# Kernel tuning notes

Hardware: AMD Instinct MI355X
Metric: run time of the kernel (lower is better)

Reference implementation:

```python
import jax, jax.numpy as jnp
import numpy as np

B = 8192          # batch_size = len(embedds)
D = 512           # ll_p['num_channels'][-1]
C = 100           # n_classes
N_LAB = 4096      # int(B * plb), plb = 0.5
MAX_ITER = 30     # gtg_i
TOL = 1e-3        # gtg_t
ENT_EPS = 1e-20


def _mlp(x, W1, b1, W2, b2, W3, b3, Wc, bc):
    h = jax.nn.relu(x @ W1 + b1)
    h = jax.nn.relu(h @ W2 + b2)
    h = jax.nn.relu(h @ W3 + b3)
    return (h @ Wc + bc)[:, 0]  # squeeze -> [B]


def _entropy(X):
    # per-row Shannon entropy (bits), as in ALGTG utils
    return -jnp.sum(X * jnp.log2(X + ENT_EPS), axis=1)


def _gtg_entropy_hist(embedds, labels):
    # get_A: cos_sim -> zero diagonal -> clamp [0,1] -> 'mean' threshold -> 'diversity' (1-A)
    n = jnp.maximum(jnp.linalg.norm(embedds, axis=-1, keepdims=True), 1e-12)
    E = embedds / n
    A = E @ E.T                                   # [B,B]
    A = A * (1.0 - jnp.eye(B, dtype=A.dtype))     # fill_diagonal_(0)
    A = jnp.clip(A, 0.0, 1.0)
    A = jnp.where(A < jnp.mean(A), 0.0, A)        # AM_threshold_strategy == 'mean'
    A = 1.0 - A                                   # AM_strategy == 'diversity'

    # get_X: labeled rows one-hot, unlabeled rows uniform 1/C
    lab = jnp.arange(B) < N_LAB
    X0 = jnp.where(lab[:, None],
                   jax.nn.one_hot(labels, C, dtype=jnp.float32),
                   jnp.full((B, C), 1.0 / C, jnp.float32))
    hist0 = jnp.zeros((B, MAX_ITER), jnp.float32)
    unlab = ~lab

    def cond(s):
        _X, _h, i, err = s
        return (err > TOL) & (i < MAX_ITER)

    def body(s):
        X, hist, i, _err = s
        Xn = X * (A @ X)                          # replicator dynamics step
        Xn = Xn / jnp.sum(Xn, axis=1, keepdims=True)
        ent = _entropy(Xn)
        hist = hist.at[:, i].set(jnp.where(unlab, ent, 0.0))
        return (Xn, hist, i + 1, jnp.linalg.norm(Xn - X))

    init = (X0, hist0, jnp.array(0, jnp.int32), jnp.array(jnp.inf, jnp.float32))
    _, hist, _, _ = jax.lax.while_loop(cond, body, init)
    return hist


def setup_inputs() -> dict:
    key = jax.random.key(0)
    ks = jax.random.split(key, 11)
    d2, d4, d8 = D // 2, D // 4, D // 8

    def lin(k, fi, fo):
        return jax.random.normal(k, (fi, fo), jnp.float32) / np.float32(np.sqrt(fi))

    return {
        'features': jax.random.normal(ks[0], (B, 64), jnp.float32),
        'embedds': jax.random.normal(ks[1], (B, D), jnp.float32),
        'labels': jax.random.randint(ks[2], (B,), 0, C),
        'W1': lin(ks[3], D, d2), 'b1': jnp.zeros((d2,), jnp.float32),
        'W2': lin(ks[4], d2, d4), 'b2': jnp.zeros((d4,), jnp.float32),
        'W3': lin(ks[5], d4, d8), 'b3': jnp.zeros((d8,), jnp.float32),
        'Wc': lin(ks[6], d8, 1), 'bc': jnp.zeros((1,), jnp.float32),
    }


def reference(features, embedds, labels, W1, b1, W2, b2, W3, b3, Wc, bc):
    y_pred = _mlp(embedds, W1, b1, W2, b2, W3, b3, Wc, bc)        # [B]
    hist = _gtg_entropy_hist(embedds, labels)                      # [B, MAX_ITER]
    y_true = jnp.mean(hist, axis=1)                                # ent_strategy == 'mean'
    labeled_mask = jnp.arange(B) < N_LAB                           # bool [B]
    return (y_pred, y_true, labeled_mask)
```

## Files before the change

kernel.cpp:

```cpp
#include <hip/hip_runtime.h>
#include <hip/hip_bf16.h>
#include <math.h>

namespace {
constexpr int BROWS = 8192;
constexpr int NLAB  = 4096;
constexpr int NUNL  = 4096;
constexpr int CREAL = 100;
constexpr int CPAD  = 112;
constexpr int DIM   = 512;
constexpr int MAXIT = 30;

constexpr size_t MiB = 1ull << 20;
constexpr size_t OFF_S    = 0;
constexpr size_t OFF_AU   = 64 * MiB;
constexpr size_t OFF_EB   = 96 * MiB;
constexpr size_t OFF_XT0  = 96 * MiB;
constexpr size_t OFF_XT1  = 98 * MiB;
constexpr size_t OFF_XU   = 100 * MiB;
constexpr size_t OFF_PL   = 102 * MiB;
constexpr size_t OFF_HIST = 104 * MiB;
constexpr size_t OFF_ERR  = 104 * MiB + 16384;
constexpr size_t OFF_MS   = 104 * MiB + 16768;
constexpr size_t OFF_RN   = 104 * MiB + 32768;
constexpr size_t MEMSET_LEN = 20480;
}

typedef __attribute__((ext_vector_type(8))) short short8;
typedef __attribute__((ext_vector_type(4))) float floatx4;

__device__ inline ushort f2bf(float f) {
  __hip_bfloat16 h = __float2bfloat16(f);
  union { __hip_bfloat16 b; ushort u; } c; c.b = h; return c.u;
}
__device__ inline float bf2f(ushort u) {
  union { ushort u; __hip_bfloat16 b; } c; c.u = u;
  return __bfloat162float(c.b);
}

__global__ __launch_bounds__(64) void k_prep(const float* __restrict__ emb,
                                             ushort* __restrict__ Eb,
                                             float* __restrict__ rn) {
  int row = blockIdx.x, l = threadIdx.x;
  const float4* e4 = (const float4*)(emb + (size_t)row * DIM);
  float4 a = e4[2 * l], b = e4[2 * l + 1];
  float f[8] = {a.x, a.y, a.z, a.w, b.x, b.y, b.z, b.w};
  float s = 0.f;
#pragma unroll
  for (int q = 0; q < 8; q++) s += f[q] * f[q];
#pragma unroll
  for (int m = 1; m < 64; m <<= 1) s += __shfl_xor(s, m);
  if (l == 0) rn[row] = 1.0f / fmaxf(sqrtf(s), 1e-12f);
  union { short8 v; ushort u[8]; } o;
#pragma unroll
  for (int q = 0; q < 8; q++) o.u[q] = f2bf(f[q]);
  *(short8*)(Eb + (size_t)row * DIM + l * 8) = o.v;
}

__global__ __launch_bounds__(256) void k_initX(ushort* __restrict__ X0,
                                               ushort* __restrict__ X1,
                                               float* __restrict__ Xu,
                                               const int* __restrict__ labels) {
  int j = blockIdx.x * 256 + threadIdx.x;
  int c = blockIdx.y;
  float v;
  if (j < NLAB) v = (labels[j] == c) ? 1.0f : 0.0f;
  else          v = (c < CREAL) ? 0.01f : 0.0f;
  ushort b = f2bf(v);
  X0[(size_t)c * BROWS + j] = b;
  X1[(size_t)c * BROWS + j] = b;
  if (j >= NLAB) Xu[(size_t)(j - NLAB) * CPAD + c] = (c < CREAL) ? 0.01f : 0.0f;
}

__global__ __launch_bounds__(256) void k_mlp(const float* __restrict__ emb,
                                             const float* __restrict__ W1, const float* __restrict__ b1,
                                             const float* __restrict__ W2, const float* __restrict__ b2,
                                             const float* __restrict__ W3, const float* __restrict__ b3,
                                             const float* __restrict__ Wc, const float* __restrict__ bc,
                                             float* __restrict__ out) {
  __shared__ float xs[4][512];
  __shared__ float h1[4][256];
  __shared__ float h2[4][128];
  __shared__ float h3[4][64];
  int t = threadIdx.x;
  int r0 = blockIdx.x * 4;
  {
    const float4* src = (const float4*)(emb + (size_t)r0 * DIM);
    float4* dst = (float4*)&xs[0][0];
    dst[t] = src[t];
    dst[t + 256] = src[t + 256];
  }
  __syncthreads();
  {
    float a0 = 0.f, a1 = 0.f, a2 = 0.f, a3 = 0.f;
    for (int k = 0; k < 512; k++) {
      float w = W1[k * 256 + t];
      a0 = fmaf(xs[0][k], w, a0);
      a1 = fmaf(xs[1][k], w, a1);
      a2 = fmaf(xs[2][k], w, a2);
      a3 = fmaf(xs[3][k], w, a3);
    }
    float bb = b1[t];
    h1[0][t] = fmaxf(a0 + bb, 0.f);
    h1[1][t] = fmaxf(a1 + bb, 0.f);
    h1[2][t] = fmaxf(a2 + bb, 0.f);
    h1[3][t] = fmaxf(a3 + bb, 0.f);
  }
  __syncthreads();
  {
    int c = t & 127, rb = (t >> 7) * 2;
    float a0 = 0.f, a1 = 0.f;
    for (int k = 0; k < 256; k++) {
      float w = W2[k * 128 + c];
      a0 = fmaf(h1[rb][k], w, a0);
      a1 = fmaf(h1[rb + 1][k], w, a1);
    }
    float bb = b2[c];
    h2[rb][c] = fmaxf(a0 + bb, 0.f);
    h2[rb + 1][c] = fmaxf(a1 + bb, 0.f);
  }
  __syncthreads();
  {
    int c = t & 63, r = t >> 6;
    float a = 0.f;
    for (int k = 0; k < 128; k++) a = fmaf(h2[r][k], W3[k * 64 + c], a);
    h3[r][c] = fmaxf(a + b3[c], 0.f);
  }
  __syncthreads();
  {
    int r = t >> 6, l = t & 63;
    float v = h3[r][l] * Wc[l];
#pragma unroll
    for (int m = 32; m; m >>= 1) v += __shfl_down(v, m);
    if (l == 0) out[r0 + r] = v + bc[0];
  }
}

__global__ __launch_bounds__(256) void k_simM(const ushort* __restrict__ Eb,
                                              const float* __restrict__ rn,
                                              ushort* __restrict__ S,
                                              double* __restrict__ meansum) {
  int x = blockIdx.x, y = blockIdx.y;
  if (x < 32 && y > x) return;
  __shared__ float redbuf[4];

  int t = threadIdx.x;
  int w = t >> 6, lane = t & 63;
  int m = lane & 15, g = lane >> 4;
  int ib = (w >> 1) * 64, jb = (w & 1) * 64;
  int i0 = x * 128, j0 = y * 128;

  floatx4 acc[4][4];
#pragma unroll
  for (int a = 0; a < 4; a++)
#pragma unroll
    for (int b = 0; b < 4; b++) acc[a][b] = (floatx4)0.0f;

  const ushort* Ei = Eb + (size_t)(i0 + ib + m) * DIM + g * 8;
  const ushort* Ej = Eb + (size_t)(j0 + jb + m) * DIM + g * 8;

  for (int kt = 0; kt < DIM; kt += 32) {
    short8 ah[4], bh[4];
#pragma unroll
    for (int rt = 0; rt < 4; rt++) ah[rt] = *(const short8*)(Ei + (size_t)(rt * 16) * DIM + kt);
#pragma unroll
    for (int ct = 0; ct < 4; ct++) bh[ct] = *(const short8*)(Ej + (size_t)(ct * 16) * DIM + kt);
#pragma unroll
    for (int rt = 0; rt < 4; rt++)
#pragma unroll
      for (int ct = 0; ct < 4; ct++)
        acc[rt][ct] = __builtin_amdgcn_mfma_f32_16x16x32_bf16(ah[rt], bh[ct], acc[rt][ct], 0, 0, 0);
  }

  bool dostore = (x >= 32);
  bool isdiag  = (x == y);
  float weight = (x < 32) ? (isdiag ? 1.0f : 2.0f) : ((y < 32) ? 2.0f : 1.0f);
  float lsum = 0.f;
#pragma unroll
  for (int rt = 0; rt < 4; rt++) {
    int gi0 = i0 + ib + rt * 16 + g * 4;
    float4 rni = *(const float4*)(rn + gi0);
#pragma unroll
    for (int ct = 0; ct < 4; ct++) {
      int gj = j0 + jb + ct * 16 + m;
      float rnj = rn[gj];
#pragma unroll
      for (int r = 0; r < 4; r++) {
        int gi = gi0 + r;
        float rv = (r == 0) ? rni.x : (r == 1) ? rni.y : (r == 2) ? rni.z : rni.w;
        float s = acc[rt][ct][r] * rv * rnj;
        if (isdiag && gi == gj) s = 0.f;
        s = fminf(fmaxf(s, 0.f), 1.f);
        lsum += s;
        if (dostore) S[(size_t)(gi - NLAB) * BROWS + gj] = f2bf(s);
      }
    }
  }
  lsum *= weight;
#pragma unroll
  for (int d = 1; d < 64; d <<= 1) lsum += __shfl_xor(lsum, d);
  if (lane == 0) redbuf[w] = lsum;
  __syncthreads();
  if (t == 0) atomicAdd(meansum, (double)(redbuf[0] + redbuf[1] + redbuf[2] + redbuf[3]));
}

__global__ __launch_bounds__(1024, 4) void k_iter(const ushort* __restrict__ S,
                                                  ushort* __restrict__ Au,
                                                  const ushort* __restrict__ XTr,
                                                  ushort* __restrict__ XTw,
                                                  float* __restrict__ Xu,
                                                  float* __restrict__ Plab,
                                                  float* __restrict__ hist,
                                                  float* __restrict__ errsq,
                                                  const double* __restrict__ ms,
                                                  int it) {
  if (it > 0 && errsq[it - 1] <= 1e-6f) return;
  __shared__ float part[8][16 * 113];
  __shared__ float Pbuf[16 * 114];
  __shared__ float dsqbuf[16];
  int t = threadIdx.x;
  int w = t >> 6, lane = t & 63;
  int m = lane & 15, g = lane >> 4;
  int r0 = blockIdx.x * 16;

  floatx4 acc[7];
#pragma unroll
  for (int c = 0; c < 7; c++) acc[c] = (floatx4)0.0f;

  if (it == 0) {
    float mean = (float)(ms[0] * (1.0 / ((double)BROWS * (double)BROWS)));
    int kw = w * 512;
    for (int ks = 0; ks < 16; ks++) {
      int kk = kw + ks * 32;
      size_t so = (size_t)(r0 + m) * BROWS + kk + g * 8;
      short8 a = __builtin_nontemporal_load((const short8*)(S + so));
      union { short8 v; ushort u[8]; } ua; ua.v = a;
#pragma unroll
      for (int e = 0; e < 8; e++) {
        float s = bf2f(ua.u[e]);
        float av = (s < mean) ? 1.0f : 1.0f - s;
        ua.u[e] = f2bf(av);
      }
      a = ua.v;
      if (w >= 8)
        *(short8*)(Au + (size_t)(r0 + m) * NUNL + (kk - NLAB) + g * 8) = a;
#pragma unroll
      for (int ct = 0; ct < 7; ct++) {
        short8 b = *(const short8*)(XTr + (size_t)(ct * 16 + m) * BROWS + kk + g * 8);
        acc[ct] = __builtin_amdgcn_mfma_f32_16x16x32_bf16(a, b, acc[ct], 0, 0, 0);
      }
    }
  } else {
    int kw = w * 256;
    size_t abase = (size_t)(r0 + m) * NUNL + kw + g * 8;
    size_t bbase = (size_t)m * BROWS + NLAB + kw + g * 8;
    short8 aC = __builtin_nontemporal_load((const short8*)(Au + abase));
    for (int ks = 0; ks < 8; ks++) {
      short8 aN;
      if (ks < 7) aN = __builtin_nontemporal_load((const short8*)(Au + abase + (ks + 1) * 32));
#pragma unroll
      for (int ct = 0; ct < 7; ct++) {
        short8 b = *(const short8*)(XTr + bbase + (size_t)ct * 16 * BROWS + ks * 32);
        acc[ct] = __builtin_amdgcn_mfma_f32_16x16x32_bf16(aC, b, acc[ct], 0, 0, 0);
      }
      aC = aN;
    }
  }

  if (w < 8) {
#pragma unroll
    for (int ct = 0; ct < 7; ct++)
#pragma unroll
      for (int r = 0; r < 4; r++)
        part[w][(g * 4 + r) * 113 + ct * 16 + m] = acc[ct][r];
  }
  __syncthreads();
  float sA[2] = {0.f, 0.f}, sB[2] = {0.f, 0.f};
#pragma unroll
  for (int q = 0; q < 2; q++) {
    int idx = t + q * 1024;
    if (idx < 16 * CPAD) {
      int row = idx / CPAD, col = idx % CPAD;
      int o = row * 113 + col;
      sA[q] = ((part[0][o] + part[1][o]) + (part[2][o] + part[3][o]))
            + ((part[4][o] + part[5][o]) + (part[6][o] + part[7][o]));
    }
  }
  __syncthreads();
  if (w >= 8) {
#pragma unroll
    for (int ct = 0; ct < 7; ct++)
#pragma unroll
      for (int r = 0; r < 4; r++)
        part[w - 8][(g * 4 + r) * 113 + ct * 16 + m] = acc[ct][r];
  }
  __syncthreads();
#pragma unroll
  for (int q = 0; q < 2; q++) {
    int idx = t + q * 1024;
    if (idx < 16 * CPAD) {
      int row = idx / CPAD, col = idx % CPAD;
      int o = row * 113 + col;
      sB[q] = ((part[0][o] + part[1][o]) + (part[2][o] + part[3][o]))
            + ((part[4][o] + part[5][o]) + (part[6][o] + part[7][o]));
      float P;
      size_t go = (size_t)(r0 + row) * CPAD + col;
      if (it == 0) { Plab[go] = sA[q]; P = sA[q] + sB[q]; }
      else         { P = sA[q] + sB[q] + Plab[go]; }
      Pbuf[row * 114 + col] = P;
    }
  }
  __syncthreads();

  int gr = r0 + w;
  bool act = lane < 56;
  float2 p = make_float2(0.f, 0.f), xo = make_float2(0.f, 0.f);
  if (act) {
    p = *(const float2*)&Pbuf[w * 114 + lane * 2];
    xo = *(const float2*)(Xu + (size_t)gr * CPAD + lane * 2);
  }
  float2 xn;
  xn.x = xo.x * p.x;
  xn.y = xo.y * p.y;
  float s = xn.x + xn.y;
#pragma unroll
  for (int d = 1; d < 64; d <<= 1) s += __shfl_xor(s, d);
  float inv = 1.0f / s;
  float ent = 0.f, dsq = 0.f;
  if (act) {
    xn.x *= inv; xn.y *= inv;
    ent = -(xn.x * log2f(xn.x + 1e-20f) + xn.y * log2f(xn.y + 1e-20f));
    float dx = xn.x - xo.x, dy = xn.y - xo.y;
    dsq = dx * dx + dy * dy;
    *(float2*)(Xu + (size_t)gr * CPAD + lane * 2) = xn;
    int c0 = lane * 2, jg = NLAB + gr;
    XTw[(size_t)c0 * BROWS + jg]       = f2bf(xn.x);
    XTw[(size_t)(c0 + 1) * BROWS + jg] = f2bf(xn.y);
  }
#pragma unroll
  for (int d = 1; d < 64; d <<= 1) { ent += __shfl_xor(ent, d); dsq += __shfl_xor(dsq, d); }
  if (lane == 0) {
    hist[gr] += ent;
    dsqbuf[w] = dsq;
  }
  __syncthreads();
  if (t == 0) {
    float ds = 0.f;
#pragma unroll
    for (int i = 0; i < 16; i++) ds += dsqbuf[i];
    atomicAdd(&errsq[it], ds);
  }
}

__global__ __launch_bounds__(256) void k_final(const float* __restrict__ hist,
                                               float* __restrict__ out) {
  int i = blockIdx.x * 256 + threadIdx.x;
  float yt = (i < NLAB) ? 0.0f : hist[i - NLAB] * (1.0f / 30.0f);
  out[BROWS + i] = yt;
  out[2 * BROWS + i] = (i < NLAB) ? 1.0f : 0.0f;
}

extern "C" void kernel_launch(void* const* d_in, const int* in_sizes, int n_in,
                              void* d_out, int out_size, void* d_ws, size_t ws_size,
                              hipStream_t stream) {
  const float* emb    = (const float*)d_in[1];
  const int*   labels = (const int*)d_in[2];
  const float* W1 = (const float*)d_in[3];
  const float* b1 = (const float*)d_in[4];
  const float* W2 = (const float*)d_in[5];
  const float* b2 = (const float*)d_in[6];
  const float* W3 = (const float*)d_in[7];
  const float* b3 = (const float*)d_in[8];
  const float* Wc = (const float*)d_in[9];
  const float* bc = (const float*)d_in[10];
  float* out = (float*)d_out;

  char* ws = (char*)d_ws;
  ushort* S    = (ushort*)(ws + OFF_S);
  ushort* Au   = (ushort*)(ws + OFF_AU);
  ushort* Eb   = (ushort*)(ws + OFF_EB);
  ushort* XT0  = (ushort*)(ws + OFF_XT0);
  ushort* XT1  = (ushort*)(ws + OFF_XT1);
  float*  Xu   = (float*)(ws + OFF_XU);
  float*  Plab = (float*)(ws + OFF_PL);
  float*  hist = (float*)(ws + OFF_HIST);
  float*  errs = (float*)(ws + OFF_ERR);
  double* ms   = (double*)(ws + OFF_MS);
  float*  rn   = (float*)(ws + OFF_RN);

  hipMemsetAsync(ws + OFF_HIST, 0, MEMSET_LEN, stream);

  k_prep<<<BROWS, 64, 0, stream>>>(emb, Eb, rn);
  k_mlp<<<BROWS / 4, 256, 0, stream>>>(emb, W1, b1, W2, b2, W3, b3, Wc, bc, out);

  { dim3 g(BROWS / 128, BROWS / 128); k_simM<<<g, 256, 0, stream>>>(Eb, rn, S, ms); }

  { dim3 g(BROWS / 256, CPAD); k_initX<<<g, 256, 0, stream>>>(XT0, XT1, Xu, labels); }

  for (int it = 0; it < MAXIT; it++) {
    const ushort* XTr = (it & 1) ? XT1 : XT0;
    ushort*       XTw = (it & 1) ? XT0 : XT1;
    k_iter<<<NUNL / 16, 1024, 0, stream>>>(S, Au, XTr, XTw, Xu, Plab, hist, errs, ms, it);
  }

  k_final<<<BROWS / 256, 256, 0, stream>>>(hist, out);
}
```

Baseline: 841.1 us.

## Stage similarity GEMM tiles through double-buffered LDS; drop nontemporal loads in GTG

The similarity kernel now loads each 128x32 bf16 tile of E once per block into padded, double-buffered shared memory and overlaps the next global load with the MFMAs. Before, each wave fetched its operands straight from global memory, repeating loads across waves. Separately, the GTG iteration kernel switches its S/Au loads from nontemporal to ordinary loads and removes the manual register prefetch of the next A fragment. This adds a block-wide barrier per k-step and uses about 40KB of LDS, which may reduce occupancy.

```diff
diff --git a/kernel.cpp b/kernel.cpp
--- a/kernel.cpp
+++ b/kernel.cpp
@@ -142,6 +142,8 @@
                                               double* __restrict__ meansum) {
   int x = blockIdx.x, y = blockIdx.y;
   if (x < 32 && y > x) return;
+  __shared__ ushort Ei[2][128 * 40];
+  __shared__ ushort Ej[2][128 * 40];
   __shared__ float redbuf[4];
 
   int t = threadIdx.x;
@@ -156,20 +158,43 @@
 #pragma unroll
     for (int b = 0; b < 4; b++) acc[a][b] = (floatx4)0.0f;
 
-  const ushort* Ei = Eb + (size_t)(i0 + ib + m) * DIM + g * 8;
-  const ushort* Ej = Eb + (size_t)(j0 + jb + m) * DIM + g * 8;
-
-  for (int kt = 0; kt < DIM; kt += 32) {
+  int lrow = t >> 1, lhalf = (t & 1) * 16;
+  const ushort* gib = Eb + (size_t)(i0 + lrow) * DIM + lhalf;
+  const ushort* gjb = Eb + (size_t)(j0 + lrow) * DIM + lhalf;
+  int o = lrow * 40 + lhalf;
+
+  short8 ri0 = *(const short8*)gib;
+  short8 ri1 = *(const short8*)(gib + 8);
+  short8 rj0 = *(const short8*)gjb;
+  short8 rj1 = *(const short8*)(gjb + 8);
+  *(short8*)&Ei[0][o] = ri0; *(short8*)&Ei[0][o + 8] = ri1;
+  *(short8*)&Ej[0][o] = rj0; *(short8*)&Ej[0][o + 8] = rj1;
+  __syncthreads();
+
+  for (int c = 0; c < 16; c++) {
+    int p = c & 1;
+    if (c < 15) {
+      int kt = (c + 1) * 32;
+      ri0 = *(const short8*)(gib + kt);
+      ri1 = *(const short8*)(gib + kt + 8);
+      rj0 = *(const short8*)(gjb + kt);
+      rj1 = *(const short8*)(gjb + kt + 8);
+    }
     short8 ah[4], bh[4];
 #pragma unroll
-    for (int rt = 0; rt < 4; rt++) ah[rt] = *(const short8*)(Ei + (size_t)(rt * 16) * DIM + kt);
-#pragma unroll
-    for (int ct = 0; ct < 4; ct++) bh[ct] = *(const short8*)(Ej + (size_t)(ct * 16) * DIM + kt);
+    for (int rt = 0; rt < 4; rt++) ah[rt] = *(const short8*)&Ei[p][(ib + rt * 16 + m) * 40 + g * 8];
+#pragma unroll
+    for (int ct = 0; ct < 4; ct++) bh[ct] = *(const short8*)&Ej[p][(jb + ct * 16 + m) * 40 + g * 8];
 #pragma unroll
     for (int rt = 0; rt < 4; rt++)
 #pragma unroll
       for (int ct = 0; ct < 4; ct++)
         acc[rt][ct] = __builtin_amdgcn_mfma_f32_16x16x32_bf16(ah[rt], bh[ct], acc[rt][ct], 0, 0, 0);
+    if (c < 15) {
+      *(short8*)&Ei[p ^ 1][o] = ri0; *(short8*)&Ei[p ^ 1][o + 8] = ri1;
+      *(short8*)&Ej[p ^ 1][o] = rj0; *(short8*)&Ej[p ^ 1][o + 8] = rj1;
+    }
+    __syncthreads();
   }
 
   bool dostore = (x >= 32);
@@ -233,7 +258,7 @@
     for (int ks = 0; ks < 16; ks++) {
       int kk = kw + ks * 32;
       size_t so = (size_t)(r0 + m) * BROWS + kk + g * 8;
-      short8 a = __builtin_nontemporal_load((const short8*)(S + so));
+      short8 a = *(const short8*)(S + so);
       union { short8 v; ushort u[8]; } ua; ua.v = a;
 #pragma unroll
       for (int e = 0; e < 8; e++) {
@@ -254,16 +279,13 @@
     int kw = w * 256;
     size_t abase = (size_t)(r0 + m) * NUNL + kw + g * 8;
     size_t bbase = (size_t)m * BROWS + NLAB + kw + g * 8;
-    short8 aC = __builtin_nontemporal_load((const short8*)(Au + abase));
     for (int ks = 0; ks < 8; ks++) {
-      short8 aN;
-      if (ks < 7) aN = __builtin_nontemporal_load((const short8*)(Au + abase + (ks + 1) * 32));
+      short8 a = *(const short8*)(Au + abase + ks * 32);
 #pragma unroll
       for (int ct = 0; ct < 7; ct++) {
         short8 b = *(const short8*)(XTr + bbase + (size_t)ct * 16 * BROWS + ks * 32);
-        acc[ct] = __builtin_amdgcn_mfma_f32_16x16x32_bf16(aC, b, acc[ct], 0, 0, 0);
+        acc[ct] = __builtin_amdgcn_mfma_f32_16x16x32_bf16(a, b, acc[ct], 0, 0, 0);
       }
-      aC = aN;
     }
   }
 
```

After: 725.8 us. 13.7% less time.
